# Performance work log

Hardware: AMD Instinct MI355X
Metric: run time of the kernel (lower is better)

## Reference

```python
import jax, jax.numpy as jnp
import numpy as np

KH, KW = 3, 3
STRIDE = 1
PADDING = 1
CIN, COUT = 64, 64


def setup_inputs() -> dict:
    key = jax.random.key(0)
    kx, kw, kb = jax.random.split(key, 3)
    x = jax.random.normal(kx, (16, CIN, 112, 112), dtype=jnp.float32)
    # Kaiming-uniform style init, matching the torch module
    fan = CIN * KH * KW
    gain = np.sqrt(2.0)
    bound_w = np.sqrt(3.0) * gain / np.sqrt(fan)
    weights = jax.random.uniform(kw, (COUT, CIN, KH, KW), dtype=jnp.float32,
                                 minval=-bound_w, maxval=bound_w)
    bound_b = 1.0 / np.sqrt(fan)
    bias = jax.random.uniform(kb, (COUT,), dtype=jnp.float32,
                              minval=-bound_b, maxval=bound_b)
    return {"x": x, "weights": weights, "bias": bias}


def reference(x, weights, bias):
    # Equivalent to F.unfold + GEMM: a standard cross-correlation conv.
    # x: (N, C, H, W), weights: (F, C, KH, KW) -> out: (N, F, H', W')
    out = jax.lax.conv_general_dilated(
        x, weights,
        window_strides=(STRIDE, STRIDE),
        padding=((PADDING, PADDING), (PADDING, PADDING)),
        dimension_numbers=("NCHW", "OIHW", "NCHW"),
    )
    return out + bias[None, :, None, None]
```

## Files before the change

kernel.cpp:

```cpp
#include <hip/hip_runtime.h>


typedef __attribute__((ext_vector_type(8))) short bf16x8;
typedef __attribute__((ext_vector_type(4))) float f32x4;

#define CIN 64
#define COUT 64
#define HH 112
#define WW 112

#define XP 72
#define WCOLS 114
#define LDS_SHORTS (3 * WCOLS * XP)
#define OP 113

__device__ __forceinline__ unsigned short f2bf(float f) {
    unsigned u = __builtin_bit_cast(unsigned, f);
    u += 0x7FFFu + ((u >> 16) & 1u);
    return (unsigned short)(u >> 16);
}

__global__ void conv_wprep(const float* __restrict__ w, short* __restrict__ wbf) {
    int i = blockIdx.x * 256 + threadIdx.x;
    int j = i & 7;
    int f = (i >> 3) & 63;
    int koct = (i >> 9) & 3;
    int cb = (i >> 11) & 1;
    int t = i >> 12;
    int c = cb * 32 + koct * 8 + j;
    int ky = t / 3, kx = t - ky * 3;
    wbf[i] = (short)f2bf(w[((f * CIN + c) * 3 + ky) * 3 + kx]);
}

__global__ __launch_bounds__(256, 3)
void conv3x3_mfma(const float* __restrict__ x, const short* __restrict__ wbf,
                  const float* __restrict__ bias, float* __restrict__ out)
{
    __shared__ __align__(16) short lds[LDS_SHORTS];
    const int tid = threadIdx.x;
    const int h = blockIdx.x;
    const int n = blockIdx.y;

    if (tid < 192) {
        int dy = tid / 64;
        int rest = tid - dy * 64;
        int wcol = (rest >= 32) ? (WCOLS - 1) : 0;
        int c2 = rest & 31;
        *(unsigned*)&lds[(dy * WCOLS + wcol) * XP + c2 * 2] = 0u;
    }
    if (h == 0) {
        for (int i = tid; i < WCOLS * 32; i += 256) {
            int wcol = i >> 5, c2 = i & 31;
            *(unsigned*)&lds[(0 * WCOLS + wcol) * XP + c2 * 2] = 0u;
        }
    }
    if (h == HH - 1) {
        for (int i = tid; i < WCOLS * 32; i += 256) {
            int wcol = i >> 5, c2 = i & 31;
            *(unsigned*)&lds[(2 * WCOLS + wcol) * XP + c2 * 2] = 0u;
        }
    }
    for (int i = tid; i < 96 * 28; i += 256) {
        int rp = i / 28;
        int w4 = i - rp * 28;
        int dy = rp >> 5;
        int c = (rp & 31) * 2;
        int gh = h + dy - 1;
        if ((unsigned)gh < (unsigned)HH) {
            const float* px = x + (((n * CIN + c) * HH + gh) * WW + w4 * 4);
            const float4 v0 = *(const float4*)px;
            const float4 v1 = *(const float4*)(px + HH * WW);
            int base = (dy * WCOLS + 1 + w4 * 4) * XP + c;
            unsigned p0 = (unsigned)f2bf(v0.x) | ((unsigned)f2bf(v1.x) << 16);
            unsigned p1 = (unsigned)f2bf(v0.y) | ((unsigned)f2bf(v1.y) << 16);
            unsigned p2 = (unsigned)f2bf(v0.z) | ((unsigned)f2bf(v1.z) << 16);
            unsigned p3 = (unsigned)f2bf(v0.w) | ((unsigned)f2bf(v1.w) << 16);
            *(unsigned*)&lds[base         ] = p0;
            *(unsigned*)&lds[base + XP    ] = p1;
            *(unsigned*)&lds[base + 2 * XP] = p2;
            *(unsigned*)&lds[base + 3 * XP] = p3;
        }
    }
    __syncthreads();

    const int wave = tid >> 6;
    const int lane = tid & 63;
    const int lm = lane & 15;
    const int lk = (lane >> 4) << 3;

    const short* wlane = wbf + ((lane >> 4) * 512 + (wave * 16 + lm) * 8);

    f32x4 acc[7];
#pragma unroll
    for (int mt = 0; mt < 7; ++mt) acc[mt] = (f32x4){0.f, 0.f, 0.f, 0.f};

#pragma unroll
    for (int ky = 0; ky < 3; ++ky) {
#pragma unroll
        for (int kx = 0; kx < 3; ++kx) {
            const int t = ky * 3 + kx;
            bf16x8 b0 = *(const bf16x8*)(wlane + t * 4096);
            bf16x8 b1 = *(const bf16x8*)(wlane + t * 4096 + 2048);
#pragma unroll
            for (int mt = 0; mt < 7; ++mt) {
                int e = (ky * WCOLS + mt * 16 + lm + kx) * XP + lk;
                bf16x8 a0 = *(const bf16x8*)&lds[e];
                bf16x8 a1 = *(const bf16x8*)&lds[e + 32];
                acc[mt] = __builtin_amdgcn_mfma_f32_16x16x32_bf16(a0, b0, acc[mt], 0, 0, 0);
                acc[mt] = __builtin_amdgcn_mfma_f32_16x16x32_bf16(a1, b1, acc[mt], 0, 0, 0);
            }
        }
    }

    __syncthreads();
    float* lout = (float*)lds;
#pragma unroll
    for (int mt = 0; mt < 7; ++mt) {
#pragma unroll
        for (int r = 0; r < 4; ++r) {
            int p = mt * 16 + ((lane >> 4) << 2) + r;
            lout[(wave * 16 + lm) * OP + p] = acc[mt][r];
        }
    }
    __syncthreads();
    for (int i = tid; i < 64 * 28; i += 256) {
        int f = i / 28;
        int w4 = i - f * 28;
        float b = bias[f];
        const float* lp = lout + f * OP + w4 * 4;
        float4 v;
        v.x = lp[0] + b; v.y = lp[1] + b; v.z = lp[2] + b; v.w = lp[3] + b;
        *(float4*)(out + (((n * COUT + f) * HH + h) * WW + w4 * 4)) = v;
    }
}

extern "C" void kernel_launch(void* const* d_in, const int* in_sizes, int n_in,
                              void* d_out, int out_size, void* d_ws, size_t ws_size,
                              hipStream_t stream) {
    const float* x = (const float*)d_in[0];
    const float* w = (const float*)d_in[1];
    const float* b = (const float*)d_in[2];
    float* out = (float*)d_out;
    short* wbf = (short*)d_ws;

    conv_wprep<<<144, 256, 0, stream>>>(w, wbf);
    dim3 grid(HH, 16);
    conv3x3_mfma<<<grid, 256, 0, stream>>>(x, wbf, b, out);
}
```

Before: 133.4 us.

## Swizzle LDS input tile, widen staging stores, preload weights, reorder grid

Input staging now reads four channels per thread and writes 8-byte packed bf16 stores into an XOR-swizzled LDS layout, and the MFMA operand reads use the matching swizzle. The aim is fewer LDS bank conflicts and fewer store instructions. All nine taps of weight fragments are loaded into registers before staging so their global latency overlaps the input loads. The grid is transposed so that consecutive blocks cover different images at the same row, which changes L2 locality. The 36 extra bf16x8 registers may raise register pressure against the launch bound of three blocks per CU.

```diff
diff --git a/kernel.cpp b/kernel.cpp
--- a/kernel.cpp
+++ b/kernel.cpp
@@ -38,57 +38,72 @@
 {
     __shared__ __align__(16) short lds[LDS_SHORTS];
     const int tid = threadIdx.x;
-    const int h = blockIdx.x;
-    const int n = blockIdx.y;
-
-    if (tid < 192) {
-        int dy = tid / 64;
-        int rest = tid - dy * 64;
-        int wcol = (rest >= 32) ? (WCOLS - 1) : 0;
-        int c2 = rest & 31;
-        *(unsigned*)&lds[(dy * WCOLS + wcol) * XP + c2 * 2] = 0u;
-    }
-    if (h == 0) {
-        for (int i = tid; i < WCOLS * 32; i += 256) {
-            int wcol = i >> 5, c2 = i & 31;
-            *(unsigned*)&lds[(0 * WCOLS + wcol) * XP + c2 * 2] = 0u;
-        }
-    }
-    if (h == HH - 1) {
-        for (int i = tid; i < WCOLS * 32; i += 256) {
-            int wcol = i >> 5, c2 = i & 31;
-            *(unsigned*)&lds[(2 * WCOLS + wcol) * XP + c2 * 2] = 0u;
-        }
-    }
-    for (int i = tid; i < 96 * 28; i += 256) {
-        int rp = i / 28;
-        int w4 = i - rp * 28;
-        int dy = rp >> 5;
-        int c = (rp & 31) * 2;
-        int gh = h + dy - 1;
-        if ((unsigned)gh < (unsigned)HH) {
-            const float* px = x + (((n * CIN + c) * HH + gh) * WW + w4 * 4);
-            const float4 v0 = *(const float4*)px;
-            const float4 v1 = *(const float4*)(px + HH * WW);
-            int base = (dy * WCOLS + 1 + w4 * 4) * XP + c;
-            unsigned p0 = (unsigned)f2bf(v0.x) | ((unsigned)f2bf(v1.x) << 16);
-            unsigned p1 = (unsigned)f2bf(v0.y) | ((unsigned)f2bf(v1.y) << 16);
-            unsigned p2 = (unsigned)f2bf(v0.z) | ((unsigned)f2bf(v1.z) << 16);
-            unsigned p3 = (unsigned)f2bf(v0.w) | ((unsigned)f2bf(v1.w) << 16);
-            *(unsigned*)&lds[base         ] = p0;
-            *(unsigned*)&lds[base + XP    ] = p1;
-            *(unsigned*)&lds[base + 2 * XP] = p2;
-            *(unsigned*)&lds[base + 3 * XP] = p3;
-        }
-    }
-    __syncthreads();
+    const int n = blockIdx.x;
+    const int h = blockIdx.y;
 
     const int wave = tid >> 6;
     const int lane = tid & 63;
     const int lm = lane & 15;
-    const int lk = (lane >> 4) << 3;
+    const int q  = lane >> 4;
 
-    const short* wlane = wbf + ((lane >> 4) * 512 + (wave * 16 + lm) * 8);
+    const short* wlane = wbf + (q * 512 + (wave * 16 + lm) * 8);
+    bf16x8 bfr[9][2];
+#pragma unroll
+    for (int t = 0; t < 9; ++t) {
+        bfr[t][0] = *(const bf16x8*)(wlane + t * 4096);
+        bfr[t][1] = *(const bf16x8*)(wlane + t * 4096 + 2048);
+    }
+
+    if (tid < 96) {
+        int e = tid & 15;
+        int g = tid >> 4;
+        int dy = g >> 1;
+        int wcol = (g & 1) ? (WCOLS - 1) : 0;
+        *(uint2*)&lds[((dy * WCOLS + wcol) * 36 + e * 2) * 2] = (uint2){0u, 0u};
+    }
+    if (h == 0) {
+        for (int i = tid; i < WCOLS * 16; i += 256) {
+            int wcol = i >> 4, e = i & 15;
+            *(uint2*)&lds[((0 * WCOLS + wcol) * 36 + e * 2) * 2] = (uint2){0u, 0u};
+        }
+    }
+    if (h == HH - 1) {
+        for (int i = tid; i < WCOLS * 16; i += 256) {
+            int wcol = i >> 4, e = i & 15;
+            *(uint2*)&lds[((2 * WCOLS + wcol) * 36 + e * 2) * 2] = (uint2){0u, 0u};
+        }
+    }
+    for (int i = tid; i < 3 * 16 * 28; i += 256) {
+        int w4 = i % 28;
+        int rp = i / 28;
+        int dy = rp >> 4;
+        int cq = rp & 15;
+        int gh = h + dy - 1;
+        if ((unsigned)gh < (unsigned)HH) {
+            int c = cq * 4;
+            const float* px = x + (((n * CIN + c) * HH + gh) * WW + w4 * 4);
+            const float4 v0 = *(const float4*)px;
+            const float4 v1 = *(const float4*)(px + HH * WW);
+            const float4 v2 = *(const float4*)(px + 2 * HH * WW);
+            const float4 v3 = *(const float4*)(px + 3 * HH * WW);
+            int o = cq >> 1, p = cq & 1;
+            float a0[4] = {v0.x, v0.y, v0.z, v0.w};
+            float a1[4] = {v1.x, v1.y, v1.z, v1.w};
+            float a2[4] = {v2.x, v2.y, v2.z, v2.w};
+            float a3[4] = {v3.x, v3.y, v3.z, v3.w};
+#pragma unroll
+            for (int dw = 0; dw < 4; ++dw) {
+                int wcol = 1 + w4 * 4 + dw;
+                int swz = (wcol >> 2) & 7;
+                int dslot = 4 * (o ^ swz) + 2 * p;
+                uint2 pk;
+                pk.x = (unsigned)f2bf(a0[dw]) | ((unsigned)f2bf(a1[dw]) << 16);
+                pk.y = (unsigned)f2bf(a2[dw]) | ((unsigned)f2bf(a3[dw]) << 16);
+                *(uint2*)&lds[((dy * WCOLS + wcol) * 36 + dslot) * 2] = pk;
+            }
+        }
+    }
+    __syncthreads();
 
     f32x4 acc[7];
 #pragma unroll
@@ -99,15 +114,15 @@
 #pragma unroll
         for (int kx = 0; kx < 3; ++kx) {
             const int t = ky * 3 + kx;
-            bf16x8 b0 = *(const bf16x8*)(wlane + t * 4096);
-            bf16x8 b1 = *(const bf16x8*)(wlane + t * 4096 + 2048);
 #pragma unroll
             for (int mt = 0; mt < 7; ++mt) {
-                int e = (ky * WCOLS + mt * 16 + lm + kx) * XP + lk;
-                bf16x8 a0 = *(const bf16x8*)&lds[e];
-                bf16x8 a1 = *(const bf16x8*)&lds[e + 32];
-                acc[mt] = __builtin_amdgcn_mfma_f32_16x16x32_bf16(a0, b0, acc[mt], 0, 0, 0);
-                acc[mt] = __builtin_amdgcn_mfma_f32_16x16x32_bf16(a1, b1, acc[mt], 0, 0, 0);
+                int wcol = mt * 16 + lm + kx;
+                int swz = (wcol >> 2) & 7;
+                int base = (ky * WCOLS + wcol) * XP;
+                bf16x8 a0 = *(const bf16x8*)&lds[base + 8 * (q ^ swz)];
+                bf16x8 a1 = *(const bf16x8*)&lds[base + 8 * ((q + 4) ^ swz)];
+                acc[mt] = __builtin_amdgcn_mfma_f32_16x16x32_bf16(a0, bfr[t][0], acc[mt], 0, 0, 0);
+                acc[mt] = __builtin_amdgcn_mfma_f32_16x16x32_bf16(a1, bfr[t][1], acc[mt], 0, 0, 0);
             }
         }
     }
@@ -118,7 +133,7 @@
     for (int mt = 0; mt < 7; ++mt) {
 #pragma unroll
         for (int r = 0; r < 4; ++r) {
-            int p = mt * 16 + ((lane >> 4) << 2) + r;
+            int p = mt * 16 + (q << 2) + r;
             lout[(wave * 16 + lm) * OP + p] = acc[mt][r];
         }
     }
@@ -144,6 +159,6 @@
     short* wbf = (short*)d_ws;
 
     conv_wprep<<<144, 256, 0, stream>>>(w, wbf);
-    dim3 grid(HH, 16);
+    dim3 grid(16, HH);
     conv3x3_mfma<<<grid, 256, 0, stream>>>(x, wbf, b, out);
 }
```

New measurement: 125.3 us. 1.06x faster.
